# Kernel optimization log

Measured on AMD Instinct MI355X. Metric: run time of the kernel, lower is better.

## Reference

```python
import jax, jax.numpy as jnp
import numpy as np

D_K = 64
POS_WIN = 2.0

def setup_inputs() -> dict:
    key = jax.random.key(0)
    k1, k2, k3, k4 = jax.random.split(key, 4)
    B, H, S, D = 2, 8, 2048, D_K
    q = jax.random.normal(k1, (B, H, S, D), dtype=jnp.float32)
    k = jax.random.normal(k2, (B, H, S, D), dtype=jnp.float32)
    v = jax.random.normal(k3, (B, H, S, D), dtype=jnp.float32)
    # graph positional distances; module turns them into a Gaussian bias
    graph_attn_bias = jax.random.uniform(k4, (B, H, S, S), dtype=jnp.float32)
    return {"q": q, "k": k, "v": v, "graph_attn_bias": graph_attn_bias}

def reference(q, k, v, graph_attn_bias):
    # attn = (q / sqrt(d_k)) @ k^T  -> [B, H, Sq, Sk]
    scale = 1.0 / jnp.sqrt(jnp.float32(D_K))
    attn = jnp.einsum('bhqd,bhkd->bhqk', q * scale, k)
    # Gaussian positional bias: -0.5 * dist^2 / (0.5 * pos_win)^2
    gaussian_w = (-0.5 / (0.5 * POS_WIN) ** 2) * jnp.square(graph_attn_bias)
    attn = attn + gaussian_w
    weights = jax.nn.softmax(attn, axis=-1)  # dropout p=0.0 -> identity
    graph_out = jnp.einsum('bhqk,bhkd->bhqd', weights, v)
    return (graph_out, weights)
```

## Files before the change

### kernel.cpp

```cpp
#include <hip/hip_runtime.h>
#include <hip/hip_bf16.h>
#include <cstdint>

#define S 2048
#define D 64
#define QT 16
#define EPAD 8
#define ESTRIDE (S + EPAD)

typedef __attribute__((ext_vector_type(8))) short short8;
typedef __attribute__((ext_vector_type(4))) float floatx4;

static __device__ __forceinline__ short f2bf(float f) {
    union { float f; uint32_t u; } v; v.f = f;
    uint32_t r = (v.u + 0x7fffu + ((v.u >> 16) & 1u)) >> 16;
    return (short)r;
}
static __device__ __forceinline__ float bf2f(short s) {
    union { uint32_t u; float f; } v; v.u = ((uint32_t)(uint16_t)s) << 16;
    return v.f;
}

__global__ __launch_bounds__(256, 2)
void attn_kernel(const float* __restrict__ q,
                 const float* __restrict__ k,
                 const float* __restrict__ v,
                 const float* __restrict__ bias,
                 float* __restrict__ gout,
                 float* __restrict__ wout)
{
    __shared__ __align__(16) short Elds[QT][ESTRIDE];
    __shared__ float rowsum[QT];

    const int tid  = threadIdx.x;
    const int wv   = tid >> 6;
    const int lane = tid & 63;
    const int quad = lane >> 4;
    const int l16  = lane & 15;

    const int bh = blockIdx.x >> 7;
    const int qt = blockIdx.x & 127;
    const int q0 = qt * QT;

    if (tid < QT) rowsum[tid] = 0.0f;
    __syncthreads();

    short8 aq[2];
    {
        const float* qrow = q + ((size_t)bh * S + q0 + l16) * D;
        #pragma unroll
        for (int s = 0; s < 2; ++s) {
            const float* p = qrow + s * 32 + quad * 8;
            #pragma unroll
            for (int j = 0; j < 8; ++j) aq[s][j] = f2bf(p[j]);
        }
    }

    float psum[4] = {0.f, 0.f, 0.f, 0.f};
    for (int t = 0; t < 32; ++t) {
        const int kb = t * 64 + wv * 16;
        short8 bk[2];
        const float* krow = k + ((size_t)bh * S + kb + l16) * D;
        #pragma unroll
        for (int s = 0; s < 2; ++s) {
            const float* p = krow + s * 32 + quad * 8;
            #pragma unroll
            for (int j = 0; j < 8; ++j) bk[s][j] = f2bf(p[j]);
        }
        floatx4 c = {0.f, 0.f, 0.f, 0.f};
        c = __builtin_amdgcn_mfma_f32_16x16x32_bf16(aq[0], bk[0], c, 0, 0, 0);
        c = __builtin_amdgcn_mfma_f32_16x16x32_bf16(aq[1], bk[1], c, 0, 0, 0);
        #pragma unroll
        for (int r = 0; r < 4; ++r) {
            const int row = quad * 4 + r;
            const float b = bias[((size_t)bh * S + q0 + row) * S + kb + l16];
            const float logit = c[r] * 0.125f - 0.5f * b * b;
            const float e = __expf(logit);
            psum[r] += e;
            Elds[row][kb + l16] = f2bf(e);
        }
    }
    #pragma unroll
    for (int r = 0; r < 4; ++r) {
        float s0 = psum[r];
        s0 += __shfl_xor(s0, 1);
        s0 += __shfl_xor(s0, 2);
        s0 += __shfl_xor(s0, 4);
        s0 += __shfl_xor(s0, 8);
        if (l16 == 0) atomicAdd(&rowsum[quad * 4 + r], s0);
    }

    __syncthreads();

    {
        const int r = tid >> 4;
        const int l = tid & 15;
        const float rinv = 1.0f / rowsum[r];
        float* wrow = wout + ((size_t)bh * S + q0 + r) * S;
        #pragma unroll 4
        for (int it = 0; it < 32; ++it) {
            const int col = it * 64 + l * 4;
            floatx4 o;
            #pragma unroll
            for (int j = 0; j < 4; ++j) o[j] = bf2f(Elds[r][col + j]) * rinv;
            *(floatx4*)(wrow + col) = o;
        }
    }

    {
        floatx4 acc = {0.f, 0.f, 0.f, 0.f};
        const int dimc = wv * 16 + l16;
        const float* vcol = v + (size_t)bh * S * D + dimc;
        for (int sl = 0; sl < 64; ++sl) {
            const int sbase = sl * 32;
            short8 af = *(const short8*)&Elds[l16][sbase + quad * 8];
            short8 bf;
            #pragma unroll
            for (int j = 0; j < 8; ++j) {
                const int key = sbase + quad * 8 + j;
                bf[j] = f2bf(vcol[(size_t)key * D]);
            }
            acc = __builtin_amdgcn_mfma_f32_16x16x32_bf16(af, bf, acc, 0, 0, 0);
        }
        #pragma unroll
        for (int r = 0; r < 4; ++r) {
            const int row = quad * 4 + r;
            const float rinv = 1.0f / rowsum[row];
            gout[((size_t)bh * S + q0 + row) * D + dimc] = acc[r] * rinv;
        }
    }
}

extern "C" void kernel_launch(void* const* d_in, const int* in_sizes, int n_in,
                              void* d_out, int out_size, void* d_ws, size_t ws_size,
                              hipStream_t stream) {
    const float* q    = (const float*)d_in[0];
    const float* k    = (const float*)d_in[1];
    const float* v    = (const float*)d_in[2];
    const float* bias = (const float*)d_in[3];
    const int BH = in_sizes[0] / (S * D);
    float* gout = (float*)d_out;
    float* wout = gout + (size_t)BH * S * D;
    dim3 grid(BH * (S / QT));
    attn_kernel<<<grid, dim3(256), 0, stream>>>(q, k, v, bias, gout, wout);
}
```

Measured before the change: 671.9 us.

## Pre-convert K to bf16 and transpose V, halve query tile size

Adds two pre-kernels that convert K to bf16 and write V transposed as bf16 into the workspace. The attention kernel then loads K and V fragments as single vector reads instead of per-element strided fp32 loads with conversion. The query tile is halved to 8 rows, doubling the grid and raising the occupancy hint to 4, which leaves half the MFMA rows unused. This costs two extra launches and a workspace round trip, and the path only runs when the workspace is large enough.

```diff
diff --git a/kernel.cpp b/kernel.cpp
--- a/kernel.cpp
+++ b/kernel.cpp
@@ -1,35 +1,70 @@
 #include <hip/hip_runtime.h>
-#include <hip/hip_bf16.h>
 #include <cstdint>
 
 #define S 2048
 #define D 64
-#define QT 16
+#define QT 8
 #define EPAD 8
 #define ESTRIDE (S + EPAD)
 
 typedef __attribute__((ext_vector_type(8))) short short8;
+typedef __attribute__((ext_vector_type(4))) short short4v;
 typedef __attribute__((ext_vector_type(4))) float floatx4;
 
-static __device__ __forceinline__ short f2bf(float f) {
+static __device__ __forceinline__ unsigned short f2bf(float f) {
     union { float f; uint32_t u; } v; v.f = f;
     uint32_t r = (v.u + 0x7fffu + ((v.u >> 16) & 1u)) >> 16;
-    return (short)r;
-}
-static __device__ __forceinline__ float bf2f(short s) {
-    union { uint32_t u; float f; } v; v.u = ((uint32_t)(uint16_t)s) << 16;
+    return (unsigned short)r;
+}
+static __device__ __forceinline__ float bf2f(unsigned short s) {
+    union { uint32_t u; float f; } v; v.u = ((uint32_t)s) << 16;
     return v.f;
 }
 
-__global__ __launch_bounds__(256, 2)
+__global__ void convert_bf16_kernel(const float* __restrict__ in,
+                                    unsigned short* __restrict__ out, int n8) {
+    int i = (blockIdx.x * 256 + threadIdx.x);
+    if (i >= n8) return;
+    const float* p = in + (size_t)i * 8;
+    short8 o;
+    #pragma unroll
+    for (int j = 0; j < 8; ++j) o[j] = (short)f2bf(p[j]);
+    *(short8*)(out + (size_t)i * 8) = o;
+}
+
+__global__ void transpose_v_kernel(const float* __restrict__ v,
+                                   unsigned short* __restrict__ vt) {
+    __shared__ unsigned short tile[64][72];
+    const int tid = threadIdx.x;
+    const int bh = blockIdx.x >> 5;
+    const int s0 = (blockIdx.x & 31) * 64;
+    #pragma unroll
+    for (int rep = 0; rep < 16; ++rep) {
+        int idx = rep * 256 + tid;
+        int sl = idx >> 6, d = idx & 63;
+        tile[sl][d] = f2bf(v[((size_t)bh * S + s0 + sl) * D + d]);
+    }
+    __syncthreads();
+    #pragma unroll
+    for (int rep = 0; rep < 16; ++rep) {
+        int idx = rep * 256 + tid;
+        int d = idx >> 6, sl = idx & 63;
+        vt[((size_t)bh * D + d) * S + s0 + sl] = tile[sl][d];
+    }
+}
+
+template <bool PRE>
+__global__ __launch_bounds__(256, 4)
 void attn_kernel(const float* __restrict__ q,
                  const float* __restrict__ k,
                  const float* __restrict__ v,
                  const float* __restrict__ bias,
+                 const unsigned short* __restrict__ kb16,
+                 const unsigned short* __restrict__ vt16,
                  float* __restrict__ gout,
                  float* __restrict__ wout)
 {
-    __shared__ __align__(16) short Elds[QT][ESTRIDE];
+    __shared__ __align__(16) unsigned short Elds[QT][ESTRIDE];
     __shared__ float rowsum[QT];
 
     const int tid  = threadIdx.x;
@@ -38,8 +73,8 @@
     const int quad = lane >> 4;
     const int l16  = lane & 15;
 
-    const int bh = blockIdx.x >> 7;
-    const int qt = blockIdx.x & 127;
+    const int bh = blockIdx.x >> 8;
+    const int qt = blockIdx.x & 255;
     const int q0 = qt * QT;
 
     if (tid < QT) rowsum[tid] = 0.0f;
@@ -47,12 +82,12 @@
 
     short8 aq[2];
     {
-        const float* qrow = q + ((size_t)bh * S + q0 + l16) * D;
+        const float* qrow = q + ((size_t)bh * S + q0 + (l16 & 7)) * D;
         #pragma unroll
         for (int s = 0; s < 2; ++s) {
             const float* p = qrow + s * 32 + quad * 8;
             #pragma unroll
-            for (int j = 0; j < 8; ++j) aq[s][j] = f2bf(p[j]);
+            for (int j = 0; j < 8; ++j) aq[s][j] = (short)f2bf(p[j]);
         }
     }
 
@@ -60,49 +95,60 @@
     for (int t = 0; t < 32; ++t) {
         const int kb = t * 64 + wv * 16;
         short8 bk[2];
-        const float* krow = k + ((size_t)bh * S + kb + l16) * D;
-        #pragma unroll
-        for (int s = 0; s < 2; ++s) {
-            const float* p = krow + s * 32 + quad * 8;
-            #pragma unroll
-            for (int j = 0; j < 8; ++j) bk[s][j] = f2bf(p[j]);
+        if (PRE) {
+            const unsigned short* kr = kb16 + ((size_t)bh * S + kb + l16) * D;
+            bk[0] = *(const short8*)(kr + quad * 8);
+            bk[1] = *(const short8*)(kr + 32 + quad * 8);
+        } else {
+            const float* krow = k + ((size_t)bh * S + kb + l16) * D;
+            #pragma unroll
+            for (int s = 0; s < 2; ++s) {
+                const float* p = krow + s * 32 + quad * 8;
+                #pragma unroll
+                for (int j = 0; j < 8; ++j) bk[s][j] = (short)f2bf(p[j]);
+            }
         }
         floatx4 c = {0.f, 0.f, 0.f, 0.f};
         c = __builtin_amdgcn_mfma_f32_16x16x32_bf16(aq[0], bk[0], c, 0, 0, 0);
         c = __builtin_amdgcn_mfma_f32_16x16x32_bf16(aq[1], bk[1], c, 0, 0, 0);
+        if (quad < 2) {
+            #pragma unroll
+            for (int r = 0; r < 4; ++r) {
+                const int row = quad * 4 + r;
+                const float b = bias[((size_t)bh * S + q0 + row) * S + kb + l16];
+                const float logit = c[r] * 0.125f - 0.5f * b * b;
+                const float e = __expf(logit);
+                psum[r] += e;
+                Elds[row][kb + l16] = f2bf(e);
+            }
+        }
+    }
+    if (quad < 2) {
         #pragma unroll
         for (int r = 0; r < 4; ++r) {
-            const int row = quad * 4 + r;
-            const float b = bias[((size_t)bh * S + q0 + row) * S + kb + l16];
-            const float logit = c[r] * 0.125f - 0.5f * b * b;
-            const float e = __expf(logit);
-            psum[r] += e;
-            Elds[row][kb + l16] = f2bf(e);
-        }
-    }
-    #pragma unroll
-    for (int r = 0; r < 4; ++r) {
-        float s0 = psum[r];
-        s0 += __shfl_xor(s0, 1);
-        s0 += __shfl_xor(s0, 2);
-        s0 += __shfl_xor(s0, 4);
-        s0 += __shfl_xor(s0, 8);
-        if (l16 == 0) atomicAdd(&rowsum[quad * 4 + r], s0);
+            float s0 = psum[r];
+            s0 += __shfl_xor(s0, 1);
+            s0 += __shfl_xor(s0, 2);
+            s0 += __shfl_xor(s0, 4);
+            s0 += __shfl_xor(s0, 8);
+            if (l16 == 0) atomicAdd(&rowsum[quad * 4 + r], s0);
+        }
     }
 
     __syncthreads();
 
     {
-        const int r = tid >> 4;
-        const int l = tid & 15;
+        const int r = tid >> 5;
+        const int l = tid & 31;
         const float rinv = 1.0f / rowsum[r];
         float* wrow = wout + ((size_t)bh * S + q0 + r) * S;
         #pragma unroll 4
-        for (int it = 0; it < 32; ++it) {
-            const int col = it * 64 + l * 4;
+        for (int it = 0; it < 16; ++it) {
+            const int col = it * 128 + l * 4;
+            short4v ev = *(const short4v*)&Elds[r][col];
             floatx4 o;
             #pragma unroll
-            for (int j = 0; j < 4; ++j) o[j] = bf2f(Elds[r][col + j]) * rinv;
+            for (int j = 0; j < 4; ++j) o[j] = bf2f((unsigned short)ev[j]) * rinv;
             *(floatx4*)(wrow + col) = o;
         }
     }
@@ -110,23 +156,33 @@
     {
         floatx4 acc = {0.f, 0.f, 0.f, 0.f};
         const int dimc = wv * 16 + l16;
-        const float* vcol = v + (size_t)bh * S * D + dimc;
-        for (int sl = 0; sl < 64; ++sl) {
-            const int sbase = sl * 32;
-            short8 af = *(const short8*)&Elds[l16][sbase + quad * 8];
-            short8 bf;
-            #pragma unroll
-            for (int j = 0; j < 8; ++j) {
-                const int key = sbase + quad * 8 + j;
-                bf[j] = f2bf(vcol[(size_t)key * D]);
-            }
-            acc = __builtin_amdgcn_mfma_f32_16x16x32_bf16(af, bf, acc, 0, 0, 0);
-        }
-        #pragma unroll
-        for (int r = 0; r < 4; ++r) {
-            const int row = quad * 4 + r;
-            const float rinv = 1.0f / rowsum[row];
-            gout[((size_t)bh * S + q0 + row) * D + dimc] = acc[r] * rinv;
+        if (PRE) {
+            const unsigned short* vrow = vt16 + ((size_t)bh * D + dimc) * S;
+            for (int sl = 0; sl < 64; ++sl) {
+                const int sbase = sl * 32;
+                short8 af = *(const short8*)&Elds[l16 & 7][sbase + quad * 8];
+                short8 bfv = *(const short8*)(vrow + sbase + quad * 8);
+                acc = __builtin_amdgcn_mfma_f32_16x16x32_bf16(af, bfv, acc, 0, 0, 0);
+            }
+        } else {
+            const float* vcol = v + (size_t)bh * S * D + dimc;
+            for (int sl = 0; sl < 64; ++sl) {
+                const int sbase = sl * 32;
+                short8 af = *(const short8*)&Elds[l16 & 7][sbase + quad * 8];
+                short8 bfv;
+                #pragma unroll
+                for (int j = 0; j < 8; ++j)
+                    bfv[j] = (short)f2bf(vcol[(size_t)(sbase + quad * 8 + j) * D]);
+                acc = __builtin_amdgcn_mfma_f32_16x16x32_bf16(af, bfv, acc, 0, 0, 0);
+            }
+        }
+        if (quad < 2) {
+            #pragma unroll
+            for (int r = 0; r < 4; ++r) {
+                const int row = quad * 4 + r;
+                const float rinv = 1.0f / rowsum[row];
+                gout[((size_t)bh * S + q0 + row) * D + dimc] = acc[r] * rinv;
+            }
         }
     }
 }
@@ -141,6 +197,20 @@
     const int BH = in_sizes[0] / (S * D);
     float* gout = (float*)d_out;
     float* wout = gout + (size_t)BH * S * D;
+
+    const size_t nkv = (size_t)BH * S * D;
+    const bool pre = ws_size >= nkv * 2 * sizeof(unsigned short);
+
     dim3 grid(BH * (S / QT));
-    attn_kernel<<<grid, dim3(256), 0, stream>>>(q, k, v, bias, gout, wout);
-}
+
+    if (pre) {
+        unsigned short* kb16 = (unsigned short*)d_ws;
+        unsigned short* vt16 = kb16 + nkv;
+        int n8 = (int)(nkv / 8);
+        convert_bf16_kernel<<<(n8 + 255) / 256, 256, 0, stream>>>(k, kb16, n8);
+        transpose_v_kernel<<<BH * (S / 64), 256, 0, stream>>>(v, vt16);
+        attn_kernel<true><<<grid, dim3(256), 0, stream>>>(q, k, v, bias, kb16, vt16, gout, wout);
+    } else {
+        attn_kernel<false><<<grid, dim3(256), 0, stream>>>(q, k, v, bias, nullptr, nullptr, gout, wout);
+    }
+}
```

Result: no change. 665.1 us (-1.0%).
